# Performance work log

Measured on AMD Instinct MI355X. Metric: run time of the kernel, lower is better.

Reference implementation:

```python
import jax, jax.numpy as jnp
import numpy as np
import math

T, D, DFF, E = 4096, 1024, 2048, 8
DEPTH_RATIO = 2.0 / 4.0  # layer_idx / n_layers
P_INIT = 0.3


def setup_inputs() -> dict:
    key = jax.random.key(0)
    ks = jax.random.split(key, 6)
    bias_init = -math.log(1.0 / P_INIT - 1.0)  # logit(0.3)
    return {
        "x": jax.random.normal(ks[0], (T, D), dtype=jnp.float32),
        "W_probe": jax.random.normal(ks[1], (E, D), dtype=jnp.float32) * 0.05,
        "b_probe": jnp.full((E,), bias_init, dtype=jnp.float32),
        "W_up": jax.random.normal(ks[2], (E, DFF, D), dtype=jnp.float32) * (1.0 / math.sqrt(D)),
        "W_gate": jax.random.normal(ks[3], (E, DFF, D), dtype=jnp.float32) * (1.0 / math.sqrt(D)),
        "W_down": jax.random.normal(ks[4], (E, D, DFF), dtype=jnp.float32) * (1.0 / math.sqrt(DFF)),
        "tau_base": jnp.full((1,), bias_init, dtype=jnp.float32),
        "gamma": jnp.full((1,), 0.5, dtype=jnp.float32),
        "w_depth": jnp.full((1,), 2.0, dtype=jnp.float32),
    }


def reference(x, W_probe, b_probe, W_up, W_gate, W_down, tau_base, gamma, w_depth):
    # DepthThreshold: tau_l = tau_base + gamma * silu(w_depth * (l/L))  (logit space)
    tau = tau_base[0] + gamma[0] * jax.nn.silu(w_depth[0] * DEPTH_RATIO)
    # MicroProbe: per-expert D->1 projections -> logits [T, E]
    logits = x @ W_probe.T + b_probe
    confidence = jax.nn.sigmoid(logits)            # [T, E]
    active = (logits > tau).astype(x.dtype)        # hard routing mask [T, E]
    scale = confidence * active                    # combine weight per (token, expert)
    # sparse_expert_dispatch, SwiGLU experts (dense-equivalent math):
    up = jnp.einsum('td,efd->etf', x, W_up)        # [E, T, DFF]
    gate = jnp.einsum('td,efd->etf', x, W_gate)    # [E, T, DFF]
    h = up * jax.nn.silu(gate)                     # [E, T, DFF]
    down = jnp.einsum('etf,edf->etd', h, W_down)   # [E, T, D]
    out = jnp.einsum('etd,te->td', down, scale)    # scatter-combine over experts
    return out
```

## Files before the change

kernel.cpp:

```cpp
#include <hip/hip_runtime.h>
#include <hip/hip_bf16.h>

#define T_DIM 4096
#define D_DIM 1024
#define DFF   2048
#define E_NUM 8

typedef short short8 __attribute__((ext_vector_type(8)));
typedef float f32x4  __attribute__((ext_vector_type(4)));

__device__ __forceinline__ unsigned short f2bf(float f) {
  union { float f; unsigned u; } v; v.f = f;
  unsigned r = v.u + 0x7FFFu + ((v.u >> 16) & 1u);
  return (unsigned short)(r >> 16);
}

__device__ __forceinline__ void load_lds16(const unsigned short* g, unsigned short* l) {
  __builtin_amdgcn_global_load_lds((const __attribute__((address_space(1))) void*)g,
                                   (__attribute__((address_space(3))) void*)l, 16, 0, 0);
}

__global__ void probe_kernel(const float* __restrict__ x, const float* __restrict__ Wp,
                             const float* __restrict__ bp, const float* __restrict__ tb,
                             const float* __restrict__ gm, const float* __restrict__ wdp,
                             float* __restrict__ scale) {
  int wave = threadIdx.x >> 6;
  int lane = threadIdx.x & 63;
  int t = blockIdx.x * 4 + wave;
  const float4* xr = (const float4*)(x + (size_t)t * D_DIM);
  float4 a[4];
#pragma unroll
  for (int k = 0; k < 4; k++) a[k] = xr[k * 64 + lane];
  float z = wdp[0] * 0.5f;
  float tau = tb[0] + gm[0] * (z / (1.f + expf(-z)));
#pragma unroll
  for (int e = 0; e < E_NUM; e++) {
    const float4* wr = (const float4*)(Wp + (size_t)e * D_DIM);
    float acc = 0.f;
#pragma unroll
    for (int k = 0; k < 4; k++) {
      float4 b = wr[k * 64 + lane];
      acc += a[k].x * b.x + a[k].y * b.y + a[k].z * b.z + a[k].w * b.w;
    }
#pragma unroll
    for (int off = 32; off > 0; off >>= 1) acc += __shfl_down(acc, off);
    if (lane == 0) {
      float logit = acc + bp[e];
      scale[t * E_NUM + e] = (logit > tau) ? (1.f / (1.f + expf(-logit))) : 0.f;
    }
  }
}

__global__ void compact_kernel(const float* __restrict__ scale, int* __restrict__ idxb,
                               float* __restrict__ scsb, int* __restrict__ cntb,
                               int* __restrict__ slotOfb) {
  int e = blockIdx.x;
  for (int t = threadIdx.x; t < T_DIM; t += 256) {
    float s = scale[t * E_NUM + e];
    if (s > 0.f) {
      int slot = atomicAdd(&cntb[e], 1);
      idxb[e * T_DIM + slot] = t;
      scsb[e * T_DIM + slot] = s;
      slotOfb[e * T_DIM + t] = slot;
    }
  }
}

__global__ void cvt_kernel(const float* __restrict__ src, unsigned short* __restrict__ dst) {
  int i = blockIdx.x * 256 + threadIdx.x;
  float4 v = ((const float4*)src)[i];
  ushort4 o;
  o.x = f2bf(v.x); o.y = f2bf(v.y); o.z = f2bf(v.z); o.w = f2bf(v.w);
  ((ushort4*)dst)[i] = o;
}

__global__ void cvt_w_kernel(const float* __restrict__ wu, const float* __restrict__ wg,
                             const float* __restrict__ wdn,
                             unsigned short* __restrict__ ou, unsigned short* __restrict__ og,
                             unsigned short* __restrict__ od) {
  int m = blockIdx.y;
  size_t i = (size_t)blockIdx.x * 256 + threadIdx.x;
  const float* s = (m == 0) ? wu : (m == 1) ? wg : wdn;
  unsigned short* d = (m == 0) ? ou : (m == 1) ? og : od;
  float4 v = ((const float4*)s)[i];
  ushort4 o;
  o.x = f2bf(v.x); o.y = f2bf(v.y); o.z = f2bf(v.z); o.w = f2bf(v.w);
  ((ushort4*)d)[i] = o;
}

__global__ void cvt3_kernel(const float* __restrict__ wu, const float* __restrict__ wg,
                            const float* __restrict__ wdn,
                            unsigned short* __restrict__ ou, unsigned short* __restrict__ og,
                            unsigned short* __restrict__ od) {
  int b = blockIdx.x;
  int m = b >> 11;
  int i = (b & 2047) * 256 + threadIdx.x;
  const float* s = (m == 0) ? wu : (m == 1) ? wg : wdn;
  unsigned short* d = (m == 0) ? ou : (m == 1) ? og : od;
  float4 v = ((const float4*)s)[i];
  ushort4 o;
  o.x = f2bf(v.x); o.y = f2bf(v.y); o.z = f2bf(v.z); o.w = f2bf(v.w);
  ((ushort4*)d)[i] = o;
}

__global__ void __launch_bounds__(256, 2)
upgate_kernel(const unsigned short* __restrict__ A,
              const unsigned short* __restrict__ Bu_base,
              const unsigned short* __restrict__ Bg_base,
              size_t wstride, size_t hstride,
              const int* __restrict__ idxb, const float* __restrict__ scsb,
              const int* __restrict__ cntb, int e_base,
              unsigned short* __restrict__ H_base) {
  int x, y, z;
  if (gridDim.y == 1) {
    int wid = blockIdx.x;
    z = wid & 7;
    int i = wid >> 3;
    x = i & 31;
    y = i >> 5;
  } else {
    x = blockIdx.x; y = blockIdx.y; z = blockIdx.z;
  }
  const int e = e_base + z;
  const int rowA0 = x * 128;
  if (rowA0 >= cntb[e]) return;
  __shared__ unsigned short smem[3 * 12288];
  const unsigned short* Bu = Bu_base + (size_t)z * wstride;
  const unsigned short* Bg = Bg_base + (size_t)z * wstride;
  unsigned short* H = H_base + (size_t)z * hstride;
  const int tid = threadIdx.x;
  const int wave = tid >> 6, lane = tid & 63;
  const int quad = lane >> 4, l15 = lane & 15;
  const int wm = (wave >> 1) * 64, wn = (wave & 1) * 64;
  const int rowB0 = y * 128;

  f32x4 accU[4][4], accG[4][4];
#pragma unroll
  for (int i2 = 0; i2 < 4; i2++)
#pragma unroll
    for (int j = 0; j < 4; j++) {
      accU[i2][j] = (f32x4){0.f, 0.f, 0.f, 0.f};
      accG[i2][j] = (f32x4){0.f, 0.f, 0.f, 0.f};
    }

  const int j0 = tid, j1 = tid + 256;
  const int ar0 = rowA0 + (j0 >> 2), ar1 = rowA0 + (j1 >> 2);
  const int br0 = rowB0 + (j0 >> 2), br1 = rowB0 + (j1 >> 2);
  const int c0 = (j0 & 3) * 8, c1 = (j1 & 3) * 8;
  const int ta0 = idxb[e * T_DIM + ar0];
  const int ta1 = idxb[e * T_DIM + ar1];

#define UG_STAGE(buf, kk) do {                                                 \
    unsigned short* _b = smem + (buf) * 12288;                                 \
    load_lds16(A  + (size_t)ta0 * D_DIM + (kk) + c0, _b + j0 * 8);             \
    load_lds16(A  + (size_t)ta1 * D_DIM + (kk) + c1, _b + j1 * 8);             \
    load_lds16(Bu + (size_t)br0 * D_DIM + (kk) + c0, _b + 4096 + j0 * 8);      \
    load_lds16(Bu + (size_t)br1 * D_DIM + (kk) + c1, _b + 4096 + j1 * 8);      \
    load_lds16(Bg + (size_t)br0 * D_DIM + (kk) + c0, _b + 8192 + j0 * 8);      \
    load_lds16(Bg + (size_t)br1 * D_DIM + (kk) + c1, _b + 8192 + j1 * 8);      \
  } while (0)

  UG_STAGE(0, 0);
  UG_STAGE(1, 32);
  for (int ks = 0; ks < 32; ks++) {
    if (ks < 30) {
      UG_STAGE((ks + 2) % 3, (ks + 2) * 32);
      asm volatile("s_waitcnt vmcnt(12)" ::: "memory");
    } else if (ks == 30) {
      asm volatile("s_waitcnt vmcnt(6)" ::: "memory");
    } else {
      asm volatile("s_waitcnt vmcnt(0)" ::: "memory");
    }
    __builtin_amdgcn_sched_barrier(0);
    __builtin_amdgcn_s_barrier();
    __builtin_amdgcn_sched_barrier(0);

    unsigned short* sA = smem + (ks % 3) * 12288;
    unsigned short* sU = sA + 4096;
    unsigned short* sG = sA + 8192;
    short8 af[4], bu[4], bg[4];
#pragma unroll
    for (int mt = 0; mt < 4; mt++)
      af[mt] = *(const short8*)(sA + (wm + mt * 16 + l15) * 32 + quad * 8);
#pragma unroll
    for (int nt = 0; nt < 4; nt++) {
      bu[nt] = *(const short8*)(sU + (wn + nt * 16 + l15) * 32 + quad * 8);
      bg[nt] = *(const short8*)(sG + (wn + nt * 16 + l15) * 32 + quad * 8);
    }
#pragma unroll
    for (int mt = 0; mt < 4; mt++)
#pragma unroll
      for (int nt = 0; nt < 4; nt++) {
        accU[mt][nt] = __builtin_amdgcn_mfma_f32_16x16x32_bf16(af[mt], bu[nt], accU[mt][nt], 0, 0, 0);
        accG[mt][nt] = __builtin_amdgcn_mfma_f32_16x16x32_bf16(af[mt], bg[nt], accG[mt][nt], 0, 0, 0);
      }
    asm volatile("s_waitcnt lgkmcnt(0)" ::: "memory");
    __builtin_amdgcn_sched_barrier(0);
    __builtin_amdgcn_s_barrier();
    __builtin_amdgcn_sched_barrier(0);
  }
#undef UG_STAGE

#pragma unroll
  for (int mt = 0; mt < 4; mt++) {
#pragma unroll
    for (int r = 0; r < 4; r++) {
      int row = rowA0 + wm + mt * 16 + quad * 4 + r;
      float s = scsb[e * T_DIM + row];
#pragma unroll
      for (int nt = 0; nt < 4; nt++) {
        int col = rowB0 + wn + nt * 16 + l15;
        float u = accU[mt][nt][r];
        float g = accG[mt][nt][r];
        float h = s * u * (g / (1.f + __expf(-g)));
        H[(size_t)row * DFF + col] = f2bf(h);
      }
    }
  }
}

__global__ void __launch_bounds__(256, 2)
down_dense_kernel(const unsigned short* __restrict__ hb,
                  const unsigned short* __restrict__ wdb,
                  const int* __restrict__ slotOfb,
                  const unsigned short* __restrict__ zrow,
                  float* __restrict__ out) {
  const size_t HSZ = (size_t)T_DIM * DFF;
  const size_t WSZ = (size_t)D_DIM * DFF;
  int wid = blockIdx.x;
  int xcd = wid & 7;
  int i = wid >> 3;
  int y = i & 7;
  int xloc = i >> 3;
  int xt = xcd * 8 + xloc;
  const int rowT0 = xt * 64, rowB0 = y * 128;

  __shared__ unsigned short smem[4 * 6144];

  const int tid = threadIdx.x;
  const int wave = tid >> 6, lane = tid & 63;
  const int quad = lane >> 4, l15 = lane & 15;
  const int wn = wave * 32;

  f32x4 acc[4][2];
#pragma unroll
  for (int m = 0; m < 4; m++)
#pragma unroll
    for (int n = 0; n < 2; n++) acc[m][n] = (f32x4){0.f, 0.f, 0.f, 0.f};

  const int cA  = (tid & 3) * 8;
  const int j0 = tid, j1 = tid + 256;
  const int brB0 = j0 >> 2, brB1 = j1 >> 2;
  const int cB = (tid & 3) * 8;
  const int tA = rowT0 + (tid >> 2);

  const unsigned short* rowp[E_NUM];
#pragma unroll
  for (int e = 0; e < E_NUM; e++) {
    int s = slotOfb[e * T_DIM + tA];
    rowp[e] = (s >= 0) ? hb + (size_t)e * HSZ + (size_t)s * DFF : zrow;
  }

#define DN_STAGE(buf, ap, bp_, kk) do {                                         \
    unsigned short* _b = smem + (buf) * 6144;                                   \
    load_lds16((ap) + (kk) + cA, _b + tid * 8);                                 \
    load_lds16((bp_) + (size_t)brB0 * DFF + (kk) + cB, _b + 2048 + j0 * 8);     \
    load_lds16((bp_) + (size_t)brB1 * DFF + (kk) + cB, _b + 2048 + j1 * 8);     \
  } while (0)

  {
    const unsigned short* ap0 = rowp[0];
    const unsigned short* bp0 = wdb + (size_t)rowB0 * DFF;
    DN_STAGE(0, ap0, bp0, 0);
    DN_STAGE(1, ap0, bp0, 32);
    DN_STAGE(2, ap0, bp0, 64);
  }

#pragma unroll
  for (int e = 0; e < E_NUM; e++) {
    const unsigned short* ap  = rowp[e];
    const unsigned short* bp_ = wdb + (size_t)e * WSZ + (size_t)rowB0 * DFF;
    const unsigned short* apN = (e < 7) ? rowp[(e < 7) ? e + 1 : e] : rowp[e];
    const unsigned short* bpN = wdb + (size_t)((e < 7) ? e + 1 : e) * WSZ + (size_t)rowB0 * DFF;
    for (int ks = 0; ks < 64; ks++) {
      if (e < 7 || ks < 61) {
        if (ks < 61) DN_STAGE((ks + 3) & 3, ap,  bp_, (ks + 3) * 32);
        else         DN_STAGE((ks + 3) & 3, apN, bpN, (ks - 61) * 32);
        asm volatile("s_waitcnt vmcnt(9)" ::: "memory");
      } else if (ks == 61) {
        asm volatile("s_waitcnt vmcnt(6)" ::: "memory");
      } else if (ks == 62) {
        asm volatile("s_waitcnt vmcnt(3)" ::: "memory");
      } else {
        asm volatile("s_waitcnt vmcnt(0)" ::: "memory");
      }
      __builtin_amdgcn_sched_barrier(0);
      __builtin_amdgcn_s_barrier();
      __builtin_amdgcn_sched_barrier(0);

      unsigned short* sA = smem + (ks & 3) * 6144;
      unsigned short* sB = sA + 2048;
      short8 af[4], bf[2];
#pragma unroll
      for (int mt = 0; mt < 4; mt++)
        af[mt] = *(const short8*)(sA + (mt * 16 + l15) * 32 + quad * 8);
#pragma unroll
      for (int nt = 0; nt < 2; nt++)
        bf[nt] = *(const short8*)(sB + (wn + nt * 16 + l15) * 32 + quad * 8);
#pragma unroll
      for (int mt = 0; mt < 4; mt++)
#pragma unroll
        for (int nt = 0; nt < 2; nt++)
          acc[mt][nt] = __builtin_amdgcn_mfma_f32_16x16x32_bf16(af[mt], bf[nt], acc[mt][nt], 0, 0, 0);
      asm volatile("s_waitcnt lgkmcnt(0)" ::: "memory");
      __builtin_amdgcn_sched_barrier(0);
      __builtin_amdgcn_s_barrier();
      __builtin_amdgcn_sched_barrier(0);
    }
  }
#undef DN_STAGE

#pragma unroll
  for (int mt = 0; mt < 4; mt++) {
#pragma unroll
    for (int r = 0; r < 4; r++) {
      int row = rowT0 + mt * 16 + quad * 4 + r;
#pragma unroll
      for (int nt = 0; nt < 2; nt++) {
        int col = rowB0 + wn + nt * 16 + l15;
        out[(size_t)row * D_DIM + col] = acc[mt][nt][r];
      }
    }
  }
}

__global__ void __launch_bounds__(256, 2)
down_kernel(const unsigned short* __restrict__ A_base,
            const unsigned short* __restrict__ B_base,
            size_t hstride, size_t wstride,
            const int* __restrict__ idxb, const int* __restrict__ cntb, int e_base,
            float* __restrict__ out) {
  const int e = e_base + blockIdx.z;
  const int rowA0 = blockIdx.x * 128;
  if (rowA0 >= cntb[e]) return;
  __shared__ unsigned short smem[2 * 128 * 32];
  unsigned short* sA = smem;
  unsigned short* sB = smem + 4096;
  const unsigned short* A = A_base + (size_t)blockIdx.z * hstride;
  const unsigned short* B = B_base + (size_t)blockIdx.z * wstride;
  const int tid = threadIdx.x;
  const int wave = tid >> 6, lane = tid & 63;
  const int quad = lane >> 4, l15 = lane & 15;
  const int wm = (wave >> 1) * 64, wn = (wave & 1) * 64;
  const int rowB0 = blockIdx.y * 128;

  f32x4 acc[4][4];
#pragma unroll
  for (int i = 0; i < 4; i++)
#pragma unroll
    for (int j = 0; j < 4; j++) acc[i][j] = (f32x4){0.f, 0.f, 0.f, 0.f};

  const int j0 = tid, j1 = tid + 256;
  const int ar0 = rowA0 + (j0 >> 2), ar1 = rowA0 + (j1 >> 2);
  const int br0 = rowB0 + (j0 >> 2), br1 = rowB0 + (j1 >> 2);
  const int c0 = (j0 & 3) * 8, c1 = (j1 & 3) * 8;

  for (int k0 = 0; k0 < DFF; k0 += 32) {
    __syncthreads();
    load_lds16(A + (size_t)ar0 * DFF + k0 + c0, sA + j0 * 8);
    load_lds16(A + (size_t)ar1 * DFF + k0 + c1, sA + j1 * 8);
    load_lds16(B + (size_t)br0 * DFF + k0 + c0, sB + j0 * 8);
    load_lds16(B + (size_t)br1 * DFF + k0 + c1, sB + j1 * 8);
    __syncthreads();

    short8 af[4], bf[4];
#pragma unroll
    for (int mt = 0; mt < 4; mt++)
      af[mt] = *(const short8*)(sA + (wm + mt * 16 + l15) * 32 + quad * 8);
#pragma unroll
    for (int nt = 0; nt < 4; nt++)
      bf[nt] = *(const short8*)(sB + (wn + nt * 16 + l15) * 32 + quad * 8);
#pragma unroll
    for (int mt = 0; mt < 4; mt++)
#pragma unroll
      for (int nt = 0; nt < 4; nt++)
        acc[mt][nt] = __builtin_amdgcn_mfma_f32_16x16x32_bf16(af[mt], bf[nt], acc[mt][nt], 0, 0, 0);
  }

#pragma unroll
  for (int mt = 0; mt < 4; mt++) {
#pragma unroll
    for (int r = 0; r < 4; r++) {
      int row = rowA0 + wm + mt * 16 + quad * 4 + r;
      int tok = idxb[e * T_DIM + row];
#pragma unroll
      for (int nt = 0; nt < 4; nt++) {
        int col = rowB0 + wn + nt * 16 + l15;
        atomicAdd(&out[(size_t)tok * D_DIM + col], acc[mt][nt][r]);
      }
    }
  }
}

extern "C" void kernel_launch(void* const* d_in, const int* in_sizes, int n_in,
                              void* d_out, int out_size, void* d_ws, size_t ws_size,
                              hipStream_t stream) {
  const float* x   = (const float*)d_in[0];
  const float* Wp  = (const float*)d_in[1];
  const float* bp  = (const float*)d_in[2];
  const float* Wu  = (const float*)d_in[3];
  const float* Wg  = (const float*)d_in[4];
  const float* Wd  = (const float*)d_in[5];
  const float* tb  = (const float*)d_in[6];
  const float* gm  = (const float*)d_in[7];
  const float* wdp = (const float*)d_in[8];
  float* out = (float*)d_out;

  const size_t WSZ = (size_t)DFF * D_DIM;
  const size_t HSZ = (size_t)T_DIM * DFF;

  char* ws = (char*)d_ws;
  float* scale         = (float*)ws;
  int*   idxb          = (int*)(ws + 131072);
  float* scsb          = (float*)(ws + 262144);
  int*   slotOfb       = (int*)(ws + 393216);
  int*   cntb          = (int*)(ws + 524288);
  unsigned short* zrow = (unsigned short*)(ws + 528384);
  unsigned short* xb   = (unsigned short*)(ws + 536576);
  const size_t HEAD    = 536576;

  hipMemsetAsync(ws + 131072, 0, 262144, stream);
  hipMemsetAsync(ws + 393216, 0xFF, 131072, stream);
  hipMemsetAsync(ws + 524288, 0, 12288, stream);
  probe_kernel<<<T_DIM / 4, 256, 0, stream>>>(x, Wp, bp, tb, gm, wdp, scale);
  compact_kernel<<<E_NUM, 256, 0, stream>>>(scale, idxb, scsb, cntb, slotOfb);
  cvt_kernel<<<T_DIM * D_DIM / 1024, 256, 0, stream>>>(x, xb);

  const size_t FULL_REQ = HEAD + 8388608 + 3 * (WSZ * 2) * E_NUM + HSZ * 2 * E_NUM;
  if (ws_size >= FULL_REQ) {
    unsigned short* wub = xb + (size_t)T_DIM * D_DIM;
    unsigned short* wgb = wub + WSZ * E_NUM;
    unsigned short* wdb = wgb + WSZ * E_NUM;
    unsigned short* hb  = wdb + WSZ * E_NUM;

    dim3 gc(WSZ * E_NUM / 1024, 3);
    cvt_w_kernel<<<gc, 256, 0, stream>>>(Wu, Wg, Wd, wub, wgb, wdb);

    upgate_kernel<<<dim3(4096, 1, 1), 256, 0, stream>>>(xb, wub, wgb, WSZ, HSZ,
                                                        idxb, scsb, cntb, 0, hb);
    down_dense_kernel<<<dim3(512, 1, 1), 256, 0, stream>>>(hb, wdb, slotOfb, zrow, out);
  } else {
    hipMemsetAsync(out, 0, (size_t)T_DIM * D_DIM * sizeof(float), stream);
    unsigned short* wub = xb + (size_t)T_DIM * D_DIM;
    unsigned short* wgb = wub + WSZ;
    unsigned short* wdb = wgb + WSZ;
    unsigned short* hb  = wdb + WSZ;

    for (int e = 0; e < E_NUM; e++) {
      cvt3_kernel<<<3 * (DFF * D_DIM / 1024), 256, 0, stream>>>(
          Wu + e * WSZ, Wg + e * WSZ, Wd + e * WSZ, wub, wgb, wdb);
      dim3 g1(T_DIM / 128, DFF / 128, 1);
      upgate_kernel<<<g1, 256, 0, stream>>>(xb, wub, wgb, 0, 0, idxb, scsb, cntb, e, hb);
      dim3 g2(T_DIM / 128, D_DIM / 128, 1);
      down_kernel<<<g2, 256, 0, stream>>>(hb, wdb, 0, 0, idxb, cntb, e, out);
    }
  }
}
```

Measured before the change: 564.1 us.

## Split down projection into per-expert compact GEMM plus bf16 gather-combine kernel

Replaces the dense down kernel, which walked all 8 experts per token tile using zero rows for inactive tokens, with a per-expert GEMM over only the compacted active slots, using 128x128 tiles and a 3-stage LDS pipeline. Each expert writes its bf16 output into a scratch buffer that reuses the up-projection weight region, and a separate combine kernel gathers each token's active expert rows and sums them in fp32. This skips MFMA work and weight traffic for inactive token/expert pairs. In exchange it adds an intermediate bf16 round-trip and an extra rounding of expert outputs, plus one more kernel launch.

```diff
diff --git a/kernel.cpp b/kernel.cpp
--- a/kernel.cpp
+++ b/kernel.cpp
@@ -13,6 +13,10 @@
   union { float f; unsigned u; } v; v.f = f;
   unsigned r = v.u + 0x7FFFu + ((v.u >> 16) & 1u);
   return (unsigned short)(r >> 16);
+}
+
+__device__ __forceinline__ float bf2f(unsigned short b) {
+  union { unsigned u; float f; } v; v.u = ((unsigned)b) << 16; return v.f;
 }
 
 __device__ __forceinline__ void load_lds16(const unsigned short* g, unsigned short* l) {
@@ -220,118 +224,112 @@
 }
 
 __global__ void __launch_bounds__(256, 2)
-down_dense_kernel(const unsigned short* __restrict__ hb,
+down_slots_kernel(const unsigned short* __restrict__ hb,
                   const unsigned short* __restrict__ wdb,
-                  const int* __restrict__ slotOfb,
-                  const unsigned short* __restrict__ zrow,
-                  float* __restrict__ out) {
+                  const int* __restrict__ cntb,
+                  unsigned short* __restrict__ de) {
+  int wid = blockIdx.x;
+  const int e = wid & 7;
+  int i = wid >> 3;
+  const int x = i & 31;
+  const int y = i >> 5;
+  const int rowA0 = x * 128;
+  if (rowA0 >= cntb[e]) return;
   const size_t HSZ = (size_t)T_DIM * DFF;
   const size_t WSZ = (size_t)D_DIM * DFF;
-  int wid = blockIdx.x;
-  int xcd = wid & 7;
-  int i = wid >> 3;
-  int y = i & 7;
-  int xloc = i >> 3;
-  int xt = xcd * 8 + xloc;
-  const int rowT0 = xt * 64, rowB0 = y * 128;
-
-  __shared__ unsigned short smem[4 * 6144];
-
+  __shared__ unsigned short smem[3 * 8192];
+  const unsigned short* A = hb + (size_t)e * HSZ;
+  const unsigned short* B = wdb + (size_t)e * WSZ;
   const int tid = threadIdx.x;
   const int wave = tid >> 6, lane = tid & 63;
   const int quad = lane >> 4, l15 = lane & 15;
-  const int wn = wave * 32;
-
-  f32x4 acc[4][2];
-#pragma unroll
-  for (int m = 0; m < 4; m++)
-#pragma unroll
-    for (int n = 0; n < 2; n++) acc[m][n] = (f32x4){0.f, 0.f, 0.f, 0.f};
-
-  const int cA  = (tid & 3) * 8;
+  const int wm = (wave >> 1) * 64, wn = (wave & 1) * 64;
+  const int rowB0 = y * 128;
+
+  f32x4 acc[4][4];
+#pragma unroll
+  for (int i2 = 0; i2 < 4; i2++)
+#pragma unroll
+    for (int j = 0; j < 4; j++) acc[i2][j] = (f32x4){0.f, 0.f, 0.f, 0.f};
+
   const int j0 = tid, j1 = tid + 256;
-  const int brB0 = j0 >> 2, brB1 = j1 >> 2;
-  const int cB = (tid & 3) * 8;
-  const int tA = rowT0 + (tid >> 2);
-
-  const unsigned short* rowp[E_NUM];
+  const int ar0 = rowA0 + (j0 >> 2), ar1 = rowA0 + (j1 >> 2);
+  const int br0 = rowB0 + (j0 >> 2), br1 = rowB0 + (j1 >> 2);
+  const int c0 = (j0 & 3) * 8, c1 = (j1 & 3) * 8;
+
+#define DS_STAGE(buf, kk) do {                                                  \
+    unsigned short* _b = smem + (buf) * 8192;                                   \
+    load_lds16(A + (size_t)ar0 * DFF + (kk) + c0, _b + j0 * 8);                 \
+    load_lds16(A + (size_t)ar1 * DFF + (kk) + c1, _b + j1 * 8);                 \
+    load_lds16(B + (size_t)br0 * DFF + (kk) + c0, _b + 4096 + j0 * 8);          \
+    load_lds16(B + (size_t)br1 * DFF + (kk) + c1, _b + 4096 + j1 * 8);          \
+  } while (0)
+
+  DS_STAGE(0, 0);
+  DS_STAGE(1, 32);
+  for (int ks = 0; ks < 64; ks++) {
+    if (ks < 62) {
+      DS_STAGE((ks + 2) % 3, (ks + 2) * 32);
+      asm volatile("s_waitcnt vmcnt(8)" ::: "memory");
+    } else if (ks == 62) {
+      asm volatile("s_waitcnt vmcnt(4)" ::: "memory");
+    } else {
+      asm volatile("s_waitcnt vmcnt(0)" ::: "memory");
+    }
+    __builtin_amdgcn_sched_barrier(0);
+    __builtin_amdgcn_s_barrier();
+    __builtin_amdgcn_sched_barrier(0);
+
+    unsigned short* sA = smem + (ks % 3) * 8192;
+    unsigned short* sB = sA + 4096;
+    short8 af[4], bf[4];
+#pragma unroll
+    for (int mt = 0; mt < 4; mt++)
+      af[mt] = *(const short8*)(sA + (wm + mt * 16 + l15) * 32 + quad * 8);
+#pragma unroll
+    for (int nt = 0; nt < 4; nt++)
+      bf[nt] = *(const short8*)(sB + (wn + nt * 16 + l15) * 32 + quad * 8);
+#pragma unroll
+    for (int mt = 0; mt < 4; mt++)
+#pragma unroll
+      for (int nt = 0; nt < 4; nt++)
+        acc[mt][nt] = __builtin_amdgcn_mfma_f32_16x16x32_bf16(af[mt], bf[nt], acc[mt][nt], 0, 0, 0);
+    asm volatile("s_waitcnt lgkmcnt(0)" ::: "memory");
+    __builtin_amdgcn_sched_barrier(0);
+    __builtin_amdgcn_s_barrier();
+    __builtin_amdgcn_sched_barrier(0);
+  }
+#undef DS_STAGE
+
+#pragma unroll
+  for (int mt = 0; mt < 4; mt++) {
+#pragma unroll
+    for (int r = 0; r < 4; r++) {
+      int row = rowA0 + wm + mt * 16 + quad * 4 + r;
+#pragma unroll
+      for (int nt = 0; nt < 4; nt++) {
+        int col = rowB0 + wn + nt * 16 + l15;
+        de[((size_t)e * T_DIM + row) * D_DIM + col] = f2bf(acc[mt][nt][r]);
+      }
+    }
+  }
+}
+
+__global__ void combine_kernel(const unsigned short* __restrict__ de,
+                               const int* __restrict__ slotOfb,
+                               float* __restrict__ out) {
+  int t = blockIdx.x;
+  int d4 = threadIdx.x;
+  float4 acc = {0.f, 0.f, 0.f, 0.f};
 #pragma unroll
   for (int e = 0; e < E_NUM; e++) {
-    int s = slotOfb[e * T_DIM + tA];
-    rowp[e] = (s >= 0) ? hb + (size_t)e * HSZ + (size_t)s * DFF : zrow;
-  }
-
-#define DN_STAGE(buf, ap, bp_, kk) do {                                         \
-    unsigned short* _b = smem + (buf) * 6144;                                   \
-    load_lds16((ap) + (kk) + cA, _b + tid * 8);                                 \
-    load_lds16((bp_) + (size_t)brB0 * DFF + (kk) + cB, _b + 2048 + j0 * 8);     \
-    load_lds16((bp_) + (size_t)brB1 * DFF + (kk) + cB, _b + 2048 + j1 * 8);     \
-  } while (0)
-
-  {
-    const unsigned short* ap0 = rowp[0];
-    const unsigned short* bp0 = wdb + (size_t)rowB0 * DFF;
-    DN_STAGE(0, ap0, bp0, 0);
-    DN_STAGE(1, ap0, bp0, 32);
-    DN_STAGE(2, ap0, bp0, 64);
-  }
-
-#pragma unroll
-  for (int e = 0; e < E_NUM; e++) {
-    const unsigned short* ap  = rowp[e];
-    const unsigned short* bp_ = wdb + (size_t)e * WSZ + (size_t)rowB0 * DFF;
-    const unsigned short* apN = (e < 7) ? rowp[(e < 7) ? e + 1 : e] : rowp[e];
-    const unsigned short* bpN = wdb + (size_t)((e < 7) ? e + 1 : e) * WSZ + (size_t)rowB0 * DFF;
-    for (int ks = 0; ks < 64; ks++) {
-      if (e < 7 || ks < 61) {
-        if (ks < 61) DN_STAGE((ks + 3) & 3, ap,  bp_, (ks + 3) * 32);
-        else         DN_STAGE((ks + 3) & 3, apN, bpN, (ks - 61) * 32);
-        asm volatile("s_waitcnt vmcnt(9)" ::: "memory");
-      } else if (ks == 61) {
-        asm volatile("s_waitcnt vmcnt(6)" ::: "memory");
-      } else if (ks == 62) {
-        asm volatile("s_waitcnt vmcnt(3)" ::: "memory");
-      } else {
-        asm volatile("s_waitcnt vmcnt(0)" ::: "memory");
-      }
-      __builtin_amdgcn_sched_barrier(0);
-      __builtin_amdgcn_s_barrier();
-      __builtin_amdgcn_sched_barrier(0);
-
-      unsigned short* sA = smem + (ks & 3) * 6144;
-      unsigned short* sB = sA + 2048;
-      short8 af[4], bf[2];
-#pragma unroll
-      for (int mt = 0; mt < 4; mt++)
-        af[mt] = *(const short8*)(sA + (mt * 16 + l15) * 32 + quad * 8);
-#pragma unroll
-      for (int nt = 0; nt < 2; nt++)
-        bf[nt] = *(const short8*)(sB + (wn + nt * 16 + l15) * 32 + quad * 8);
-#pragma unroll
-      for (int mt = 0; mt < 4; mt++)
-#pragma unroll
-        for (int nt = 0; nt < 2; nt++)
-          acc[mt][nt] = __builtin_amdgcn_mfma_f32_16x16x32_bf16(af[mt], bf[nt], acc[mt][nt], 0, 0, 0);
-      asm volatile("s_waitcnt lgkmcnt(0)" ::: "memory");
-      __builtin_amdgcn_sched_barrier(0);
-      __builtin_amdgcn_s_barrier();
-      __builtin_amdgcn_sched_barrier(0);
-    }
-  }
-#undef DN_STAGE
-
-#pragma unroll
-  for (int mt = 0; mt < 4; mt++) {
-#pragma unroll
-    for (int r = 0; r < 4; r++) {
-      int row = rowT0 + mt * 16 + quad * 4 + r;
-#pragma unroll
-      for (int nt = 0; nt < 2; nt++) {
-        int col = rowB0 + wn + nt * 16 + l15;
-        out[(size_t)row * D_DIM + col] = acc[mt][nt][r];
-      }
-    }
-  }
+    int s = slotOfb[e * T_DIM + t];
+    if (s >= 0) {
+      ushort4 v = ((const ushort4*)(de + ((size_t)e * T_DIM + s) * D_DIM))[d4];
+      acc.x += bf2f(v.x); acc.y += bf2f(v.y); acc.z += bf2f(v.z); acc.w += bf2f(v.w);
+    }
+  }
+  ((float4*)(out + (size_t)t * D_DIM))[d4] = acc;
 }
 
 __global__ void __launch_bounds__(256, 2)
@@ -425,13 +423,12 @@
   float* scsb          = (float*)(ws + 262144);
   int*   slotOfb       = (int*)(ws + 393216);
   int*   cntb          = (int*)(ws + 524288);
-  unsigned short* zrow = (unsigned short*)(ws + 528384);
   unsigned short* xb   = (unsigned short*)(ws + 536576);
   const size_t HEAD    = 536576;
 
   hipMemsetAsync(ws + 131072, 0, 262144, stream);
   hipMemsetAsync(ws + 393216, 0xFF, 131072, stream);
-  hipMemsetAsync(ws + 524288, 0, 12288, stream);
+  hipMemsetAsync(ws + 524288, 0, 4096, stream);
   probe_kernel<<<T_DIM / 4, 256, 0, stream>>>(x, Wp, bp, tb, gm, wdp, scale);
   compact_kernel<<<E_NUM, 256, 0, stream>>>(scale, idxb, scsb, cntb, slotOfb);
   cvt_kernel<<<T_DIM * D_DIM / 1024, 256, 0, stream>>>(x, xb);
@@ -448,7 +445,9 @@
 
     upgate_kernel<<<dim3(4096, 1, 1), 256, 0, stream>>>(xb, wub, wgb, WSZ, HSZ,
                                                         idxb, scsb, cntb, 0, hb);
-    down_dense_kernel<<<dim3(512, 1, 1), 256, 0, stream>>>(hb, wdb, slotOfb, zrow, out);
+    unsigned short* de = wub;
+    down_slots_kernel<<<dim3(2048, 1, 1), 256, 0, stream>>>(hb, wdb, cntb, de);
+    combine_kernel<<<dim3(T_DIM, 1, 1), 256, 0, stream>>>(de, slotOfb, out);
   } else {
     hipMemsetAsync(out, 0, (size_t)T_DIM * D_DIM * sizeof(float), stream);
     unsigned short* wub = xb + (size_t)T_DIM * D_DIM;
```

After: 472.9 us. 1.19x faster.
